# Performance work log

Measured on AMD Instinct MI355X. Metric: run time of the kernel, lower is better.

Reference implementation:

```python
import jax, jax.numpy as jnp
import numpy as np

B, T, INPUT = 8, 16, 64
OUTPUT = 128
N_IN, N_TR, N_ACT = 32, 192, 32
N = N_IN + N_TR + N_ACT
H = 256   # neuron_hidden_dim
KQ = 256  # key_query_dim
S = 256   # signal_dim

def _xavier(key, shape):
    fan_in, fan_out = shape[-2], shape[-1]
    lim = np.sqrt(6.0 / (fan_in + fan_out)).astype(np.float32)
    return jax.random.uniform(key, shape, jnp.float32, -lim, lim)

def setup_inputs() -> dict:
    key = jax.random.key(0)
    ks = jax.random.split(key, 10)
    return {
        'x': jax.random.normal(ks[0], (B, T, INPUT), jnp.float32),
        'w_rec_input': _xavier(ks[1], (N_IN, INPUT, H)),
        'b_rec_input': jnp.zeros((N_IN, H), jnp.float32),
        'w_rec_other': _xavier(ks[2], (N_TR + N_ACT, S, H)),
        'b_rec_other': jnp.zeros((N_TR + N_ACT, H), jnp.float32),
        'w_lstm_ih': _xavier(ks[3], (N, H, 4 * H)),
        'b_lstm_ih': jnp.zeros((N, 4 * H), jnp.float32),
        'w_lstm_hh': _xavier(ks[4], (N, H, 4 * H)),
        'b_lstm_hh': jnp.zeros((N, 4 * H), jnp.float32),
        'w_query': _xavier(ks[5], (N, H, KQ)),
        'b_query': jnp.zeros((N, KQ), jnp.float32),
        'w_key': _xavier(ks[6], (N, H, KQ)),
        'b_key': jnp.zeros((N, KQ), jnp.float32),
        'w_sender': _xavier(ks[7], (N, H, S)),
        'b_sender': jnp.zeros((N, S), jnp.float32),
        'w_proj': _xavier(ks[8], (OUTPUT, N_ACT * S)),  # nn.Linear weight [out, in]
        'b_proj': jnp.zeros((OUTPUT,), jnp.float32),
    }

def reference(x, w_rec_input, b_rec_input, w_rec_other, b_rec_other,
              w_lstm_ih, b_lstm_ih, w_lstm_hh, b_lstm_hh,
              w_query, b_query, w_key, b_key, w_sender, b_sender,
              w_proj, b_proj):
    batch = x.shape[0]
    scale = 1.0 / np.sqrt(KQ).astype(np.float32)

    def step(carry, x_t):
        h, c, prev = carry  # [B,N,H], [B,N,H], [B,N,S]
        Q = jnp.einsum('bnh,nhk->bnk', h, w_query) + b_query
        K = jnp.einsum('bnh,nhk->bnk', h, w_key) + b_key
        scores = jnp.einsum('bnk,bmk->bnm', Q, K) * scale
        weights = jax.nn.softmax(scores, axis=2)
        ctx = jnp.einsum('bnm,bms->bns', weights, prev)  # [B,N,S]
        rec_in = jnp.einsum('bi,nih->bnh', x_t, w_rec_input) + b_rec_input  # [B,N_IN,H]
        rec_oth = jnp.einsum('bns,nsh->bnh', ctx[:, N_IN:, :], w_rec_other) + b_rec_other
        lstm_in = jax.nn.relu(jnp.concatenate([rec_in, rec_oth], axis=1))  # [B,N,H]
        gates = (jnp.einsum('bnh,nhg->bng', lstm_in, w_lstm_ih) + b_lstm_ih
                 + jnp.einsum('bnh,nhg->bng', h, w_lstm_hh) + b_lstm_hh)
        i_g, f_g, g_g, o_g = jnp.split(gates, 4, axis=2)
        c_new = jax.nn.sigmoid(f_g) * c + jax.nn.sigmoid(i_g) * jnp.tanh(g_g)
        h_new = jax.nn.sigmoid(o_g) * jnp.tanh(c_new)
        prev_new = jnp.einsum('bnh,nhs->bns', h_new, w_sender) + b_sender
        action = prev_new[:, -N_ACT:, :].reshape(batch, -1)
        out = action @ w_proj.T + b_proj
        return (h_new, c_new, prev_new), out

    init = (jnp.zeros((batch, N, H), x.dtype),
            jnp.zeros((batch, N, H), x.dtype),
            jnp.zeros((batch, N, S), x.dtype))
    _, outs = jax.lax.scan(step, init, jnp.swapaxes(x, 0, 1))  # outs: [T,B,OUTPUT]
    return jnp.swapaxes(outs, 0, 1)
```

## Files before the change

### kernel.cpp

```cpp
#include <hip/hip_runtime.h>
#include <cmath>

#define DEV_INLINE __device__ __forceinline__

constexpr int B_ = 8, T_ = 16, INPUT_ = 64, OUTPUT_ = 128;
constexpr int N_ = 256, H_ = 256, KQ_ = 256, S_ = 256, G_ = 1024;
constexpr int NIN_ = 32;
constexpr float SCALE_ = 0.0625f;

DEV_INLINE float sigmoid_(float x) { return 1.0f / (1.0f + expf(-x)); }
DEV_INLINE void fma4(float4& a, const float4& w, float s) {
    a.x += w.x * s; a.y += w.y * s; a.z += w.z * s; a.w += w.w * s;
}

__global__ __launch_bounds__(256)
void pnmm256_kernel(const float* __restrict__ in,
                    const float* __restrict__ W0, const float* __restrict__ bias0, float* __restrict__ O0,
                    const float* __restrict__ W1, const float* __restrict__ bias1, float* __restrict__ O1,
                    const float* __restrict__ W2, const float* __restrict__ bias2, float* __restrict__ O2,
                    int n0, int nW0, int relu)
{
    const int ny = blockIdx.x;
    const int n = n0 + ny;
    const int nw = n - nW0;
    const float* W; const float* bias; float* O;
    if (blockIdx.y == 0)      { W = W0; bias = bias0; O = O0; }
    else if (blockIdx.y == 1) { W = W1; bias = bias1; O = O1; }
    else                      { W = W2; bias = bias2; O = O2; }

    const int tid = threadIdx.x;
    const int wv = tid >> 6;
    const int lane = tid & 63;
    const int c0 = lane * 4;
    const int h0 = wv * 64;

    __shared__ float sh[256 * 8];
    __shared__ float psum[4][2048];

    for (int i = tid; i < 2048; i += 256) {
        int hh = i & 255, b = i >> 8;
        sh[hh * 8 + b] = in[(size_t)(b * N_ + n) * H_ + hh];
    }
    __syncthreads();

    const float* wp = W + ((size_t)nw * H_ + h0) * 256 + c0;
    float4 acc[8] = {};
    float4 bufA[8], bufB[8];
#pragma unroll
    for (int u = 0; u < 8; ++u) bufA[u] = *(const float4*)(wp + (size_t)u * 256);
#pragma unroll 1
    for (int hb = 0; hb < 64; hb += 8) {
        if (hb + 8 < 64) {
#pragma unroll
            for (int u = 0; u < 8; ++u)
                bufB[u] = *(const float4*)(wp + (size_t)(hb + 8 + u) * 256);
        }
#pragma unroll
        for (int u = 0; u < 8; ++u) {
            float4 w = bufA[u];
            const float* ip = &sh[(h0 + hb + u) * 8];
            float4 i0 = *(const float4*)ip;
            float4 i1 = *(const float4*)(ip + 4);
            fma4(acc[0], w, i0.x); fma4(acc[1], w, i0.y);
            fma4(acc[2], w, i0.z); fma4(acc[3], w, i0.w);
            fma4(acc[4], w, i1.x); fma4(acc[5], w, i1.y);
            fma4(acc[6], w, i1.z); fma4(acc[7], w, i1.w);
        }
#pragma unroll
        for (int u = 0; u < 8; ++u) bufA[u] = bufB[u];
    }
#pragma unroll
    for (int b = 0; b < 8; ++b)
        *(float4*)&psum[wv][b * 256 + c0] = acc[b];
    __syncthreads();

    for (int i = tid; i < 2048; i += 256) {
        int b = i >> 8, cc = i & 255;
        float s = psum[0][i] + psum[1][i] + psum[2][i] + psum[3][i]
                + bias[(size_t)nw * 256 + cc];
        if (relu) s = fmaxf(s, 0.f);
        O[(size_t)(b * N_ + n) * H_ + cc] = s;
    }
}

__global__ __launch_bounds__(512)
void gatescell_kernel(const float* __restrict__ lin,
                      const float* __restrict__ rec_all,
                      int t,
                      const float* __restrict__ wih, const float* __restrict__ whh,
                      const float* __restrict__ bih, const float* __restrict__ bhh,
                      float* __restrict__ c, float* __restrict__ h)
{
    const int n = blockIdx.x;
    const int tid = threadIdx.x;
    const int sp = tid >> 8;
    const int c0 = (tid & 255) * 4;
    const int h0 = sp * 128;

    __shared__ float smem[8192];
    float* shi = smem;
    float* shh = smem + 2048;
    float* glds = smem;

    for (int i = tid; i < 2048; i += 512) {
        int hh = i & 255, b = i >> 8;
        shh[hh * 8 + b] = h[(size_t)(b * N_ + n) * H_ + hh];
        shi[hh * 8 + b] = (n < NIN_)
            ? rec_all[(((size_t)t * 8 + b) * NIN_ + n) * H_ + hh]
            : lin[(size_t)(b * N_ + n) * H_ + hh];
    }
    __syncthreads();

    const float* wi = wih + ((size_t)n * H_ + h0) * G_ + c0;
    const float* wh = whh + ((size_t)n * H_ + h0) * G_ + c0;
    float4 acc[8] = {};
    float4 biA[4], bhA[4], biB[4], bhB[4];
#pragma unroll
    for (int u = 0; u < 4; ++u) {
        biA[u] = *(const float4*)(wi + (size_t)u * G_);
        bhA[u] = *(const float4*)(wh + (size_t)u * G_);
    }
#pragma unroll 1
    for (int hb = 0; hb < 128; hb += 4) {
        if (hb + 4 < 128) {
#pragma unroll
            for (int u = 0; u < 4; ++u) {
                biB[u] = *(const float4*)(wi + (size_t)(hb + 4 + u) * G_);
                bhB[u] = *(const float4*)(wh + (size_t)(hb + 4 + u) * G_);
            }
        }
#pragma unroll
        for (int u = 0; u < 4; ++u) {
            float4 a = biA[u];
            float4 hv = bhA[u];
            const float* ip = &shi[(h0 + hb + u) * 8];
            const float* hp = &shh[(h0 + hb + u) * 8];
            float4 i0 = *(const float4*)ip;
            float4 i1 = *(const float4*)(ip + 4);
            float4 h0v = *(const float4*)hp;
            float4 h1v = *(const float4*)(hp + 4);
            fma4(acc[0], a, i0.x); fma4(acc[0], hv, h0v.x);
            fma4(acc[1], a, i0.y); fma4(acc[1], hv, h0v.y);
            fma4(acc[2], a, i0.z); fma4(acc[2], hv, h0v.z);
            fma4(acc[3], a, i0.w); fma4(acc[3], hv, h0v.w);
            fma4(acc[4], a, i1.x); fma4(acc[4], hv, h1v.x);
            fma4(acc[5], a, i1.y); fma4(acc[5], hv, h1v.y);
            fma4(acc[6], a, i1.z); fma4(acc[6], hv, h1v.z);
            fma4(acc[7], a, i1.w); fma4(acc[7], hv, h1v.w);
        }
#pragma unroll
        for (int u = 0; u < 4; ++u) { biA[u] = biB[u]; bhA[u] = bhB[u]; }
    }
    __syncthreads();
    if (sp == 1) {
#pragma unroll
        for (int b = 0; b < 8; ++b)
            *(float4*)&glds[b * 1024 + c0] = acc[b];
    }
    __syncthreads();
    if (sp == 0) {
        float4 bi = *(const float4*)&bih[(size_t)n * G_ + c0];
        float4 bh = *(const float4*)&bhh[(size_t)n * G_ + c0];
#pragma unroll
        for (int b = 0; b < 8; ++b) {
            float4 g = *(const float4*)&glds[b * 1024 + c0];
            g.x += acc[b].x + bi.x + bh.x;
            g.y += acc[b].y + bi.y + bh.y;
            g.z += acc[b].z + bi.z + bh.z;
            g.w += acc[b].w + bi.w + bh.w;
            *(float4*)&glds[b * 1024 + c0] = g;
        }
    }
    __syncthreads();
#pragma unroll
    for (int e = 0; e < 4; ++e) {
        int idx = tid + 512 * e;
        int b = idx >> 8, hx = idx & 255;
        float ig = glds[b * 1024 + 0   + hx];
        float fg = glds[b * 1024 + 256 + hx];
        float gg = glds[b * 1024 + 512 + hx];
        float og = glds[b * 1024 + 768 + hx];
        size_t off = (size_t)(b * N_ + n) * H_ + hx;
        float cv = c[off];
        float cn = sigmoid_(fg) * cv + sigmoid_(ig) * tanhf(gg);
        c[off] = cn;
        h[off] = sigmoid_(og) * tanhf(cn);
    }
}

__global__ __launch_bounds__(256)
void rec_in_all_kernel(const float* __restrict__ x,
                       const float* __restrict__ w_ri, const float* __restrict__ b_ri,
                       float* __restrict__ rec_all)
{
    __shared__ float sh[INPUT_ * 8];
    const int n = blockIdx.x;
    const int t = blockIdx.y;
    const int tid = threadIdx.x;
    for (int i = tid; i < INPUT_ * 8; i += 256) {
        int hh = i & 63, b = i >> 6;
        sh[hh * 8 + b] = x[((size_t)b * T_ + t) * INPUT_ + hh];
    }
    __syncthreads();
    const float* wp = w_ri + (size_t)n * INPUT_ * H_ + tid;
    float acc[8] = {};
#pragma unroll 8
    for (int hh = 0; hh < INPUT_; ++hh) {
        float w = wp[(size_t)hh * H_];
        float4 i0 = *(const float4*)&sh[hh * 8];
        float4 i1 = *(const float4*)&sh[hh * 8 + 4];
        acc[0] += w * i0.x; acc[1] += w * i0.y; acc[2] += w * i0.z; acc[3] += w * i0.w;
        acc[4] += w * i1.x; acc[5] += w * i1.y; acc[6] += w * i1.z; acc[7] += w * i1.w;
    }
    float bv = b_ri[n * H_ + tid];
#pragma unroll
    for (int b = 0; b < 8; ++b)
        rec_all[(((size_t)t * 8 + b) * NIN_ + n) * H_ + tid] = fmaxf(acc[b] + bv, 0.f);
}

__global__ void scores_kernel(const float* __restrict__ Q, const float* __restrict__ Kb,
                              float* __restrict__ sc)
{
    __shared__ float As[16][64];
    __shared__ float Bs[16][64];
    const int b = blockIdx.y;
    const int tile = blockIdx.x;
    const int row0 = (tile >> 2) * 64;
    const int col0 = (tile & 3) * 64;
    const int tid = threadIdx.x;
    const int tx = tid & 15, ty = tid >> 4;
    const int lr = tid >> 2;
    const int kq = (tid & 3) * 4;
    const float* Qb = Q + (size_t)b * N_ * KQ_;
    const float* Kbb = Kb + (size_t)b * N_ * KQ_;
    float acc[4][4] = {};
    for (int kt = 0; kt < KQ_; kt += 16) {
        float4 av = *(const float4*)&Qb[(size_t)(row0 + lr) * KQ_ + kt + kq];
        float4 bv = *(const float4*)&Kbb[(size_t)(col0 + lr) * KQ_ + kt + kq];
        __syncthreads();
        As[kq + 0][lr] = av.x; As[kq + 1][lr] = av.y; As[kq + 2][lr] = av.z; As[kq + 3][lr] = av.w;
        Bs[kq + 0][lr] = bv.x; Bs[kq + 1][lr] = bv.y; Bs[kq + 2][lr] = bv.z; Bs[kq + 3][lr] = bv.w;
        __syncthreads();
#pragma unroll
        for (int k = 0; k < 16; ++k) {
            float4 a = *(const float4*)&As[k][ty * 4];
            float4 c = *(const float4*)&Bs[k][tx * 4];
            acc[0][0] += a.x * c.x; acc[0][1] += a.x * c.y; acc[0][2] += a.x * c.z; acc[0][3] += a.x * c.w;
            acc[1][0] += a.y * c.x; acc[1][1] += a.y * c.y; acc[1][2] += a.y * c.z; acc[1][3] += a.y * c.w;
            acc[2][0] += a.z * c.x; acc[2][1] += a.z * c.y; acc[2][2] += a.z * c.z; acc[2][3] += a.z * c.w;
            acc[3][0] += a.w * c.x; acc[3][1] += a.w * c.y; acc[3][2] += a.w * c.z; acc[3][3] += a.w * c.w;
        }
    }
#pragma unroll
    for (int i = 0; i < 4; ++i) {
        float4 r = make_float4(acc[i][0] * SCALE_, acc[i][1] * SCALE_,
                               acc[i][2] * SCALE_, acc[i][3] * SCALE_);
        *(float4*)&sc[((size_t)b * N_ + row0 + ty * 4 + i) * N_ + col0 + tx * 4] = r;
    }
}

__global__ __launch_bounds__(256)
void smctx_kernel(const float* __restrict__ sc, const float* __restrict__ prev,
                  float* __restrict__ ctx)
{
    __shared__ float Ws[256][68];
    __shared__ float Bs[16][64];
    __shared__ float redm[4][64];
    __shared__ float reds[4][64];
    __shared__ float rmax[64];
    __shared__ float rinv[64];

    const int b = blockIdx.y;
    const int tile = blockIdx.x;
    const int row0 = (tile >> 2) * 64;
    const int col0 = (tile & 3) * 64;
    const int tid = threadIdx.x;
    const int r = tid & 63;
    const int q = tid >> 6;

    const float* srow = sc + ((size_t)b * N_ + row0 + r) * N_ + q * 64;
    float lmax = -3.4e38f;
#pragma unroll
    for (int i = 0; i < 16; ++i) {
        float4 v = *(const float4*)&srow[4 * i];
        Ws[q * 64 + 4 * i + 0][r] = v.x;
        Ws[q * 64 + 4 * i + 1][r] = v.y;
        Ws[q * 64 + 4 * i + 2][r] = v.z;
        Ws[q * 64 + 4 * i + 3][r] = v.w;
        lmax = fmaxf(lmax, fmaxf(fmaxf(v.x, v.y), fmaxf(v.z, v.w)));
    }
    redm[q][r] = lmax;
    __syncthreads();
    if (tid < 64)
        rmax[tid] = fmaxf(fmaxf(redm[0][tid], redm[1][tid]),
                          fmaxf(redm[2][tid], redm[3][tid]));
    __syncthreads();
    {
        float m = rmax[r];
        float lsum = 0.f;
#pragma unroll 4
        for (int i = 0; i < 64; ++i) {
            float e = expf(Ws[q * 64 + i][r] - m);
            Ws[q * 64 + i][r] = e;
            lsum += e;
        }
        reds[q][r] = lsum;
    }
    __syncthreads();
    if (tid < 64)
        rinv[tid] = 1.0f / (reds[0][tid] + reds[1][tid] + reds[2][tid] + reds[3][tid]);

    const int tx = tid & 15, ty = tid >> 4;
    const int br = tid >> 4, bc = (tid & 15) * 4;
    float acc[4][4] = {};
    for (int kt = 0; kt < N_; kt += 16) {
        float4 bv = *(const float4*)&prev[((size_t)b * N_ + kt + br) * S_ + col0 + bc];
        __syncthreads();
        *(float4*)&Bs[br][bc] = bv;
        __syncthreads();
#pragma unroll
        for (int k = 0; k < 16; ++k) {
            float4 a = *(const float4*)&Ws[kt + k][ty * 4];
            float4 c = *(const float4*)&Bs[k][tx * 4];
            acc[0][0] += a.x * c.x; acc[0][1] += a.x * c.y; acc[0][2] += a.x * c.z; acc[0][3] += a.x * c.w;
            acc[1][0] += a.y * c.x; acc[1][1] += a.y * c.y; acc[1][2] += a.y * c.z; acc[1][3] += a.y * c.w;
            acc[2][0] += a.z * c.x; acc[2][1] += a.z * c.y; acc[2][2] += a.z * c.z; acc[2][3] += a.z * c.w;
            acc[3][0] += a.w * c.x; acc[3][1] += a.w * c.y; acc[3][2] += a.w * c.z; acc[3][3] += a.w * c.w;
        }
    }
#pragma unroll
    for (int i = 0; i < 4; ++i) {
        float inv = rinv[ty * 4 + i];
        float4 rr = make_float4(acc[i][0] * inv, acc[i][1] * inv,
                                acc[i][2] * inv, acc[i][3] * inv);
        *(float4*)&ctx[((size_t)b * N_ + row0 + ty * 4 + i) * S_ + col0 + tx * 4] = rr;
    }
}

__global__ __launch_bounds__(64)
void proj64_kernel(const float* __restrict__ prev, const float* __restrict__ wp,
                   const float* __restrict__ bp, float* __restrict__ out, int t)
{
    const int o = blockIdx.x;
    const int lane = threadIdx.x;
    const float* wr = wp + (size_t)o * (NIN_ * S_);
    float acc[8] = {};
    for (int i = lane * 4; i < NIN_ * S_; i += 256) {
        float4 w = *(const float4*)&wr[i];
#pragma unroll
        for (int b = 0; b < 8; ++b) {
            float4 p = *(const float4*)&prev[((size_t)b * N_ + (N_ - NIN_)) * S_ + i];
            acc[b] += w.x * p.x + w.y * p.y + w.z * p.z + w.w * p.w;
        }
    }
#pragma unroll
    for (int b = 0; b < 8; ++b)
        for (int off = 32; off > 0; off >>= 1)
            acc[b] += __shfl_down(acc[b], off);
    if (lane == 0) {
        float bv = bp[o];
#pragma unroll
        for (int b = 0; b < 8; ++b)
            out[((size_t)b * T_ + t) * OUTPUT_ + o] = acc[b] + bv;
    }
}

extern "C" void kernel_launch(void* const* d_in, const int* in_sizes, int n_in,
                              void* d_out, int out_size, void* d_ws, size_t ws_size,
                              hipStream_t stream)
{
    (void)in_sizes; (void)n_in; (void)out_size; (void)ws_size;
    const float* x    = (const float*)d_in[0];
    const float* w_ri = (const float*)d_in[1];
    const float* b_ri = (const float*)d_in[2];
    const float* w_ro = (const float*)d_in[3];
    const float* b_ro = (const float*)d_in[4];
    const float* w_ih = (const float*)d_in[5];
    const float* b_ih = (const float*)d_in[6];
    const float* w_hh = (const float*)d_in[7];
    const float* b_hh = (const float*)d_in[8];
    const float* w_q  = (const float*)d_in[9];
    const float* b_q  = (const float*)d_in[10];
    const float* w_k  = (const float*)d_in[11];
    const float* b_k  = (const float*)d_in[12];
    const float* w_s  = (const float*)d_in[13];
    const float* b_s  = (const float*)d_in[14];
    const float* w_p  = (const float*)d_in[15];
    const float* b_p  = (const float*)d_in[16];
    float* out = (float*)d_out;

    float* ws = (float*)d_ws;
    const size_t SZ = (size_t)B_ * N_ * H_;
    float* hbuf = ws;
    float* cbuf = hbuf + SZ;
    float* prev = cbuf + SZ;
    float* Q    = prev + SZ;
    float* Kb   = Q + SZ;
    float* sc   = Kb + SZ;
    float* ctxb = sc + SZ;
    float* lin  = ctxb + SZ;
    float* rec_all = lin + SZ;

    hipMemsetAsync(d_ws, 0, 3 * SZ * sizeof(float), stream);

    rec_in_all_kernel<<<dim3(NIN_, T_), 256, 0, stream>>>(x, w_ri, b_ri, rec_all);
    pnmm256_kernel<<<dim3(256, 2), 256, 0, stream>>>(hbuf,
        w_q, b_q, Q, w_k, b_k, Kb, w_k, b_k, Kb, 0, 0, 0);

    for (int t = 0; t < T_; ++t) {
        scores_kernel<<<dim3(16, B_), 256, 0, stream>>>(Q, Kb, sc);
        smctx_kernel<<<dim3(16, B_), 256, 0, stream>>>(sc, prev, ctxb);
        pnmm256_kernel<<<dim3(224, 1), 256, 0, stream>>>(ctxb,
            w_ro, b_ro, lin, w_ro, b_ro, lin, w_ro, b_ro, lin, NIN_, NIN_, 1);
        gatescell_kernel<<<dim3(256), 512, 0, stream>>>(lin, rec_all, t,
            w_ih, w_hh, b_ih, b_hh, cbuf, hbuf);
        pnmm256_kernel<<<dim3(256, 3), 256, 0, stream>>>(hbuf,
            w_s, b_s, prev, w_q, b_q, Q, w_k, b_k, Kb, 0, 0, 0);
        proj64_kernel<<<dim3(OUTPUT_), 64, 0, stream>>>(prev, w_p, b_p, out, t);
    }
}
```

Baseline: 3.922 ms.

## Fuse per-neuron rec_other, LSTM gates, and sender/query/key projections into one kernel

Merges the three per-step kernels (rec_other matmul, gates+cell, and the sender/Q/K projections) into a single neuron_step kernel with one 512-thread block per neuron. The intermediates (lin and h_new) stay in shared memory instead of going through global memory, and two launches per timestep are removed. The initial Q/K computation from a zero hidden state is replaced by a broadcast of the biases. The trade-off is less parallelism: the output projections now run as 256 blocks doing three sequential matmuls with scalar loads, where the separate launch used 768 blocks with float4 loads.

Measured after the change: 3.893 ms. Within noise of the previous version (-0.7%).

```diff
diff --git a/kernel.cpp b/kernel.cpp
--- a/kernel.cpp
+++ b/kernel.cpp
@@ -13,145 +13,168 @@
     a.x += w.x * s; a.y += w.y * s; a.z += w.z * s; a.w += w.w * s;
 }
 
-__global__ __launch_bounds__(256)
-void pnmm256_kernel(const float* __restrict__ in,
-                    const float* __restrict__ W0, const float* __restrict__ bias0, float* __restrict__ O0,
-                    const float* __restrict__ W1, const float* __restrict__ bias1, float* __restrict__ O1,
-                    const float* __restrict__ W2, const float* __restrict__ bias2, float* __restrict__ O2,
-                    int n0, int nW0, int relu)
-{
-    const int ny = blockIdx.x;
-    const int n = n0 + ny;
-    const int nw = n - nW0;
-    const float* W; const float* bias; float* O;
-    if (blockIdx.y == 0)      { W = W0; bias = bias0; O = O0; }
-    else if (blockIdx.y == 1) { W = W1; bias = bias1; O = O1; }
-    else                      { W = W2; bias = bias2; O = O2; }
-
-    const int tid = threadIdx.x;
-    const int wv = tid >> 6;
-    const int lane = tid & 63;
-    const int c0 = lane * 4;
-    const int h0 = wv * 64;
-
-    __shared__ float sh[256 * 8];
-    __shared__ float psum[4][2048];
-
-    for (int i = tid; i < 2048; i += 256) {
-        int hh = i & 255, b = i >> 8;
-        sh[hh * 8 + b] = in[(size_t)(b * N_ + n) * H_ + hh];
-    }
-    __syncthreads();
-
-    const float* wp = W + ((size_t)nw * H_ + h0) * 256 + c0;
-    float4 acc[8] = {};
-    float4 bufA[8], bufB[8];
-#pragma unroll
-    for (int u = 0; u < 8; ++u) bufA[u] = *(const float4*)(wp + (size_t)u * 256);
+DEV_INLINE void out_mm256(int n, int tid, const float* __restrict__ W,
+                          const float* __restrict__ bias, float* __restrict__ O,
+                          const float* hnew, float* psum0, float* psum1)
+{
+    const int hcol = tid & 255;
+    const int sp = tid >> 8;
+    const float* wp = W + ((size_t)n * H_ + sp * 128) * 256 + hcol;
+    float acc[8] = {};
+    float wA[8], wB[8];
+#pragma unroll
+    for (int u = 0; u < 8; ++u) wA[u] = wp[(size_t)u * 256];
 #pragma unroll 1
-    for (int hb = 0; hb < 64; hb += 8) {
-        if (hb + 8 < 64) {
-#pragma unroll
-            for (int u = 0; u < 8; ++u)
-                bufB[u] = *(const float4*)(wp + (size_t)(hb + 8 + u) * 256);
+    for (int s0 = 0; s0 < 128; s0 += 8) {
+        if (s0 + 8 < 128) {
+#pragma unroll
+            for (int u = 0; u < 8; ++u) wB[u] = wp[(size_t)(s0 + 8 + u) * 256];
         }
 #pragma unroll
         for (int u = 0; u < 8; ++u) {
-            float4 w = bufA[u];
-            const float* ip = &sh[(h0 + hb + u) * 8];
+            float w = wA[u];
+            const float* ip = &hnew[(sp * 128 + s0 + u) * 8];
             float4 i0 = *(const float4*)ip;
             float4 i1 = *(const float4*)(ip + 4);
-            fma4(acc[0], w, i0.x); fma4(acc[1], w, i0.y);
-            fma4(acc[2], w, i0.z); fma4(acc[3], w, i0.w);
-            fma4(acc[4], w, i1.x); fma4(acc[5], w, i1.y);
-            fma4(acc[6], w, i1.z); fma4(acc[7], w, i1.w);
-        }
-#pragma unroll
-        for (int u = 0; u < 8; ++u) bufA[u] = bufB[u];
-    }
-#pragma unroll
-    for (int b = 0; b < 8; ++b)
-        *(float4*)&psum[wv][b * 256 + c0] = acc[b];
-    __syncthreads();
-
-    for (int i = tid; i < 2048; i += 256) {
-        int b = i >> 8, cc = i & 255;
-        float s = psum[0][i] + psum[1][i] + psum[2][i] + psum[3][i]
-                + bias[(size_t)nw * 256 + cc];
-        if (relu) s = fmaxf(s, 0.f);
-        O[(size_t)(b * N_ + n) * H_ + cc] = s;
-    }
+            acc[0] += w * i0.x; acc[1] += w * i0.y; acc[2] += w * i0.z; acc[3] += w * i0.w;
+            acc[4] += w * i1.x; acc[5] += w * i1.y; acc[6] += w * i1.z; acc[7] += w * i1.w;
+        }
+#pragma unroll
+        for (int u = 0; u < 8; ++u) wA[u] = wB[u];
+    }
+    float* dst = sp ? psum1 : psum0;
+    *(float4*)&dst[hcol * 8] = make_float4(acc[0], acc[1], acc[2], acc[3]);
+    *(float4*)&dst[hcol * 8 + 4] = make_float4(acc[4], acc[5], acc[6], acc[7]);
+    __syncthreads();
+    for (int i = tid; i < 2048; i += 512) {
+        int hh = i & 255, b = i >> 8;
+        float v = psum0[hh * 8 + b] + psum1[hh * 8 + b] + bias[(size_t)n * H_ + hh];
+        O[(size_t)(b * N_ + n) * H_ + hh] = v;
+    }
+    __syncthreads();
 }
 
 __global__ __launch_bounds__(512)
-void gatescell_kernel(const float* __restrict__ lin,
-                      const float* __restrict__ rec_all,
-                      int t,
-                      const float* __restrict__ wih, const float* __restrict__ whh,
-                      const float* __restrict__ bih, const float* __restrict__ bhh,
-                      float* __restrict__ c, float* __restrict__ h)
+void neuron_step_kernel(const float* __restrict__ ctx,
+                        const float* __restrict__ rec_all, int t,
+                        const float* __restrict__ w_ro, const float* __restrict__ b_ro,
+                        const float* __restrict__ wih, const float* __restrict__ whh,
+                        const float* __restrict__ bih, const float* __restrict__ bhh,
+                        const float* __restrict__ w_s, const float* __restrict__ b_s,
+                        const float* __restrict__ w_q, const float* __restrict__ b_q,
+                        const float* __restrict__ w_k, const float* __restrict__ b_k,
+                        float* __restrict__ c, float* __restrict__ h,
+                        float* __restrict__ prev, float* __restrict__ Q,
+                        float* __restrict__ K)
 {
     const int n = blockIdx.x;
     const int tid = threadIdx.x;
+
+    __shared__ float A[8192];
+    __shared__ float Bh[2048];
+    float* sctx  = A;
+    float* shi   = A + 2048;
+    float* shh   = A + 4096;
+    float* spare = A + 6144;
+    float* glds  = A;
+
+    for (int i = tid; i < 2048; i += 512) {
+        int hh = i & 255, b = i >> 8;
+        size_t off = (size_t)(b * N_ + n) * H_ + hh;
+        shh[hh * 8 + b] = h[off];
+        if (n < NIN_)
+            shi[hh * 8 + b] = rec_all[(((size_t)t * 8 + b) * NIN_ + n) * H_ + hh];
+        else
+            sctx[hh * 8 + b] = ctx[off];
+    }
+    __syncthreads();
+
+    if (n >= NIN_) {
+        const int hcol = tid & 255;
+        const int sp = tid >> 8;
+        const float* wp = w_ro + ((size_t)(n - NIN_) * H_ + sp * 128) * 256 + hcol;
+        float acc[8] = {};
+        float wA[8], wB[8];
+#pragma unroll
+        for (int u = 0; u < 8; ++u) wA[u] = wp[(size_t)u * 256];
+#pragma unroll 1
+        for (int s0 = 0; s0 < 128; s0 += 8) {
+            if (s0 + 8 < 128) {
+#pragma unroll
+                for (int u = 0; u < 8; ++u) wB[u] = wp[(size_t)(s0 + 8 + u) * 256];
+            }
+#pragma unroll
+            for (int u = 0; u < 8; ++u) {
+                float w = wA[u];
+                const float* ip = &sctx[(sp * 128 + s0 + u) * 8];
+                float4 i0 = *(const float4*)ip;
+                float4 i1 = *(const float4*)(ip + 4);
+                acc[0] += w * i0.x; acc[1] += w * i0.y; acc[2] += w * i0.z; acc[3] += w * i0.w;
+                acc[4] += w * i1.x; acc[5] += w * i1.y; acc[6] += w * i1.z; acc[7] += w * i1.w;
+            }
+#pragma unroll
+            for (int u = 0; u < 8; ++u) wA[u] = wB[u];
+        }
+        float* dst = sp ? spare : shi;
+        *(float4*)&dst[hcol * 8] = make_float4(acc[0], acc[1], acc[2], acc[3]);
+        *(float4*)&dst[hcol * 8 + 4] = make_float4(acc[4], acc[5], acc[6], acc[7]);
+        __syncthreads();
+        for (int i = tid; i < 2048; i += 512) {
+            int hh = i & 255, b = i >> 8;
+            float v = shi[hh * 8 + b] + spare[hh * 8 + b]
+                    + b_ro[(size_t)(n - NIN_) * H_ + hh];
+            shi[hh * 8 + b] = fmaxf(v, 0.f);
+        }
+    }
+    __syncthreads();
+
     const int sp = tid >> 8;
     const int c0 = (tid & 255) * 4;
     const int h0 = sp * 128;
-
-    __shared__ float smem[8192];
-    float* shi = smem;
-    float* shh = smem + 2048;
-    float* glds = smem;
-
-    for (int i = tid; i < 2048; i += 512) {
-        int hh = i & 255, b = i >> 8;
-        shh[hh * 8 + b] = h[(size_t)(b * N_ + n) * H_ + hh];
-        shi[hh * 8 + b] = (n < NIN_)
-            ? rec_all[(((size_t)t * 8 + b) * NIN_ + n) * H_ + hh]
-            : lin[(size_t)(b * N_ + n) * H_ + hh];
-    }
-    __syncthreads();
-
     const float* wi = wih + ((size_t)n * H_ + h0) * G_ + c0;
     const float* wh = whh + ((size_t)n * H_ + h0) * G_ + c0;
     float4 acc[8] = {};
-    float4 biA[4], bhA[4], biB[4], bhB[4];
-#pragma unroll
-    for (int u = 0; u < 4; ++u) {
-        biA[u] = *(const float4*)(wi + (size_t)u * G_);
-        bhA[u] = *(const float4*)(wh + (size_t)u * G_);
-    }
+    {
+        float4 biA[4], bhA[4], biB[4], bhB[4];
+#pragma unroll
+        for (int u = 0; u < 4; ++u) {
+            biA[u] = *(const float4*)(wi + (size_t)u * G_);
+            bhA[u] = *(const float4*)(wh + (size_t)u * G_);
+        }
 #pragma unroll 1
-    for (int hb = 0; hb < 128; hb += 4) {
-        if (hb + 4 < 128) {
+        for (int hb = 0; hb < 128; hb += 4) {
+            if (hb + 4 < 128) {
+#pragma unroll
+                for (int u = 0; u < 4; ++u) {
+                    biB[u] = *(const float4*)(wi + (size_t)(hb + 4 + u) * G_);
+                    bhB[u] = *(const float4*)(wh + (size_t)(hb + 4 + u) * G_);
+                }
+            }
 #pragma unroll
             for (int u = 0; u < 4; ++u) {
-                biB[u] = *(const float4*)(wi + (size_t)(hb + 4 + u) * G_);
-                bhB[u] = *(const float4*)(wh + (size_t)(hb + 4 + u) * G_);
+                float4 a = biA[u];
+                float4 hv = bhA[u];
+                const float* ip = &shi[(h0 + hb + u) * 8];
+                const float* hp = &shh[(h0 + hb + u) * 8];
+                float4 i0 = *(const float4*)ip;
+                float4 i1 = *(const float4*)(ip + 4);
+                float4 h0v = *(const float4*)hp;
+                float4 h1v = *(const float4*)(hp + 4);
+                fma4(acc[0], a, i0.x); fma4(acc[0], hv, h0v.x);
+                fma4(acc[1], a, i0.y); fma4(acc[1], hv, h0v.y);
+                fma4(acc[2], a, i0.z); fma4(acc[2], hv, h0v.z);
+                fma4(acc[3], a, i0.w); fma4(acc[3], hv, h0v.w);
+                fma4(acc[4], a, i1.x); fma4(acc[4], hv, h1v.x);
+                fma4(acc[5], a, i1.y); fma4(acc[5], hv, h1v.y);
+                fma4(acc[6], a, i1.z); fma4(acc[6], hv, h1v.z);
+                fma4(acc[7], a, i1.w); fma4(acc[7], hv, h1v.w);
             }
-        }
-#pragma unroll
-        for (int u = 0; u < 4; ++u) {
-            float4 a = biA[u];
-            float4 hv = bhA[u];
-            const float* ip = &shi[(h0 + hb + u) * 8];
-            const float* hp = &shh[(h0 + hb + u) * 8];
-            float4 i0 = *(const float4*)ip;
-            float4 i1 = *(const float4*)(ip + 4);
-            float4 h0v = *(const float4*)hp;
-            float4 h1v = *(const float4*)(hp + 4);
-            fma4(acc[0], a, i0.x); fma4(acc[0], hv, h0v.x);
-            fma4(acc[1], a, i0.y); fma4(acc[1], hv, h0v.y);
-            fma4(acc[2], a, i0.z); fma4(acc[2], hv, h0v.z);
-            fma4(acc[3], a, i0.w); fma4(acc[3], hv, h0v.w);
-            fma4(acc[4], a, i1.x); fma4(acc[4], hv, h1v.x);
-            fma4(acc[5], a, i1.y); fma4(acc[5], hv, h1v.y);
-            fma4(acc[6], a, i1.z); fma4(acc[6], hv, h1v.z);
-            fma4(acc[7], a, i1.w); fma4(acc[7], hv, h1v.w);
-        }
-#pragma unroll
-        for (int u = 0; u < 4; ++u) { biA[u] = biB[u]; bhA[u] = bhB[u]; }
-    }
-    __syncthreads();
+#pragma unroll
+            for (int u = 0; u < 4; ++u) { biA[u] = biB[u]; bhA[u] = bhB[u]; }
+        }
+    }
+    __syncthreads();
+
     if (sp == 1) {
 #pragma unroll
         for (int b = 0; b < 8; ++b)
@@ -183,9 +206,16 @@
         size_t off = (size_t)(b * N_ + n) * H_ + hx;
         float cv = c[off];
         float cn = sigmoid_(fg) * cv + sigmoid_(ig) * tanhf(gg);
+        float hn = sigmoid_(og) * tanhf(cn);
         c[off] = cn;
-        h[off] = sigmoid_(og) * tanhf(cn);
-    }
+        h[off] = hn;
+        Bh[hx * 8 + b] = hn;
+    }
+    __syncthreads();
+
+    out_mm256(n, tid, w_s, b_s, prev, Bh, shi, spare);
+    out_mm256(n, tid, w_q, b_q, Q,    Bh, shi, spare);
+    out_mm256(n, tid, w_k, b_k, K,    Bh, shi, spare);
 }
 
 __global__ __launch_bounds__(256)
@@ -216,6 +246,20 @@
 #pragma unroll
     for (int b = 0; b < 8; ++b)
         rec_all[(((size_t)t * 8 + b) * NIN_ + n) * H_ + tid] = fmaxf(acc[b] + bv, 0.f);
+}
+
+__global__ __launch_bounds__(256)
+void qkinit_kernel(const float* __restrict__ b_q, const float* __restrict__ b_k,
+                   float* __restrict__ Q, float* __restrict__ K)
+{
+    const int idx = (blockIdx.x * 256 + threadIdx.x) * 4;
+    float4 qv = *(const float4*)&b_q[idx];
+    float4 kv = *(const float4*)&b_k[idx];
+#pragma unroll
+    for (int b = 0; b < 8; ++b) {
+        *(float4*)&Q[(size_t)b * N_ * KQ_ + idx] = qv;
+        *(float4*)&K[(size_t)b * N_ * KQ_ + idx] = kv;
+    }
 }
 
 __global__ void scores_kernel(const float* __restrict__ Q, const float* __restrict__ Kb,
@@ -398,24 +442,20 @@
     float* Kb   = Q + SZ;
     float* sc   = Kb + SZ;
     float* ctxb = sc + SZ;
-    float* lin  = ctxb + SZ;
-    float* rec_all = lin + SZ;
+    float* rec_all = ctxb + SZ;
 
     hipMemsetAsync(d_ws, 0, 3 * SZ * sizeof(float), stream);
 
     rec_in_all_kernel<<<dim3(NIN_, T_), 256, 0, stream>>>(x, w_ri, b_ri, rec_all);
-    pnmm256_kernel<<<dim3(256, 2), 256, 0, stream>>>(hbuf,
-        w_q, b_q, Q, w_k, b_k, Kb, w_k, b_k, Kb, 0, 0, 0);
+    qkinit_kernel<<<dim3(64), 256, 0, stream>>>(b_q, b_k, Q, Kb);
 
     for (int t = 0; t < T_; ++t) {
         scores_kernel<<<dim3(16, B_), 256, 0, stream>>>(Q, Kb, sc);
         smctx_kernel<<<dim3(16, B_), 256, 0, stream>>>(sc, prev, ctxb);
-        pnmm256_kernel<<<dim3(224, 1), 256, 0, stream>>>(ctxb,
-            w_ro, b_ro, lin, w_ro, b_ro, lin, w_ro, b_ro, lin, NIN_, NIN_, 1);
-        gatescell_kernel<<<dim3(256), 512, 0, stream>>>(lin, rec_all, t,
-            w_ih, w_hh, b_ih, b_hh, cbuf, hbuf);
-        pnmm256_kernel<<<dim3(256, 3), 256, 0, stream>>>(hbuf,
-            w_s, b_s, prev, w_q, b_q, Q, w_k, b_k, Kb, 0, 0, 0);
+        neuron_step_kernel<<<dim3(N_), 512, 0, stream>>>(ctxb, rec_all, t,
+            w_ro, b_ro, w_ih, w_hh, b_ih, b_hh,
+            w_s, b_s, w_q, b_q, w_k, b_k,
+            cbuf, hbuf, prev, Q, Kb);
         proj64_kernel<<<dim3(OUTPUT_), 64, 0, stream>>>(prev, w_p, b_p, out, t);
     }
 }
```
